# Optimization experiments

Measured on AMD Instinct MI355X. Metric: run time of the kernel, lower is better.

The kernel has to match this reference:

```python
import jax, jax.numpy as jnp
import numpy as np

# Pulse convention: bits[..., k] = bit k (LSB-first) of the IEEE-754 binary16 word.
# bits 0..9 = mantissa, bits 10..14 = exponent, bit 15 = sign.

def _encode_fp16(y16):
    """float16 array -> pulse bits [..., 16] in float32 {0,1}."""
    u = jax.lax.bitcast_convert_type(y16, jnp.uint16)
    k = jnp.arange(16, dtype=jnp.uint16)
    return ((u[..., None] >> k) & jnp.uint16(1)).astype(jnp.float32)

def _decode_fp16(bits):
    """Pulse bits [..., 16] -> exact fp16 value as float32 (arithmetic decode)."""
    pm = jnp.asarray([float(2 ** i) for i in range(10)], jnp.float32)
    pe = jnp.asarray([1.0, 2.0, 4.0, 8.0, 16.0], jnp.float32)
    m = bits[..., :10] @ pm          # mantissa integer [0, 1023]
    e = bits[..., 10:15] @ pe        # biased exponent [0, 31]
    s = 1.0 - 2.0 * bits[..., 15]    # sign
    frac = m * (1.0 / 1024.0)
    # normal: (-1)^s * 2^(e-15) * (1 + m/1024); subnormal (e==0): (-1)^s * 2^-14 * m/1024
    val = jnp.where(e > 0.0, jnp.exp2(e - 15.0) * (1.0 + frac), jnp.exp2(-14.0) * frac)
    return s * val

def setup_inputs() -> dict:
    key = jax.random.key(0)
    kx, kw = jax.random.split(key)
    B, T, IN, OUT = 4, 256, 512, 512
    x = jax.random.normal(kx, (B, T, IN), jnp.float32).astype(jnp.float16)
    w = (jax.random.normal(kw, (OUT, IN), jnp.float32) * (IN ** -0.5)).astype(jnp.float16)
    return {"x_pulse": _encode_fp16(x), "w_pulse": _encode_fp16(w)}

def reference(x_pulse, w_pulse):
    # x_pulse: [B, T, in, 16]; w_pulse: [out, in, 16]
    x_val = _decode_fp16(x_pulse)    # [B, T, in] exact fp16 values in fp32
    w_val = _decode_fp16(w_pulse)    # [out, in]
    # SpikeFP16MulToFP32: fp16*fp16 -> fp32 is exact (22-bit product fits fp32).
    # SequentialAccumulator: bit-exact deterministic O(n) fp32 add, i = 0..in-1.
    xs = (jnp.moveaxis(x_val, -1, 0), w_val.T)   # ([in, B, T], [in, out])
    acc0 = jnp.zeros(x_val.shape[:-1] + (w_val.shape[0],), jnp.float32)  # [B, T, out]
    def step(acc, xw):
        xi, wi = xw                   # [B, T], [out]
        return acc + xi[..., None] * wi, None
    acc, _ = jax.lax.scan(step, acc0, xs)
    # FP32ToFP16Converter (round-to-nearest-even) then re-encode to pulses.
    return _encode_fp16(acc.astype(jnp.float16))   # [B, T, out, 16]
```

## Files before the change

### kernel.cpp

```cpp
#include <hip/hip_runtime.h>
#include <hip/hip_fp16.h>

constexpr int K    = 512;
constexpr int ROWS = 1024;
constexpr int COLS = 512;
constexpr int NX   = ROWS * K;
constexpr int NW   = COLS * K;

__global__ __launch_bounds__(256) void decode_k(const float* __restrict__ xp,
                                                const float* __restrict__ wp,
                                                float* __restrict__ dec) {
    const int e = blockIdx.x * 256 + threadIdx.x;
    const float4* s4;
    if (e < NX) s4 = (const float4*)(xp + (size_t)e * 16);
    else        s4 = (const float4*)(wp + (size_t)(e - NX) * 16);
    const float4 v0 = s4[0];
    const float4 v1 = s4[1];
    const float4 v2 = s4[2];
    const float4 v3 = s4[3];
    unsigned u = 0;
    u |= (unsigned)(v0.x > 0.5f) << 0;
    u |= (unsigned)(v0.y > 0.5f) << 1;
    u |= (unsigned)(v0.z > 0.5f) << 2;
    u |= (unsigned)(v0.w > 0.5f) << 3;
    u |= (unsigned)(v1.x > 0.5f) << 4;
    u |= (unsigned)(v1.y > 0.5f) << 5;
    u |= (unsigned)(v1.z > 0.5f) << 6;
    u |= (unsigned)(v1.w > 0.5f) << 7;
    u |= (unsigned)(v2.x > 0.5f) << 8;
    u |= (unsigned)(v2.y > 0.5f) << 9;
    u |= (unsigned)(v2.z > 0.5f) << 10;
    u |= (unsigned)(v2.w > 0.5f) << 11;
    u |= (unsigned)(v3.x > 0.5f) << 12;
    u |= (unsigned)(v3.y > 0.5f) << 13;
    u |= (unsigned)(v3.z > 0.5f) << 14;
    u |= (unsigned)(v3.w > 0.5f) << 15;
    dec[e] = __half2float(__ushort_as_half((unsigned short)u));
}

__global__ __launch_bounds__(256) void gemm_k(const float* __restrict__ dec,
                                              float* __restrict__ out) {
    const float* __restrict__ xv = dec;
    const float* __restrict__ wv = dec + NX;

    __shared__ float Bs[64][68];

    const int tid  = threadIdx.x;
    const int lane = tid & 63;
    const int wid  = __builtin_amdgcn_readfirstlane(tid >> 6);
    const int col0 = blockIdx.x * 64;
    const int row0 = blockIdx.y * 32 + wid * 8;

    float acc[8] = {0.f, 0.f, 0.f, 0.f, 0.f, 0.f, 0.f, 0.f};

    const int scol = tid >> 2;
    const int skq  = (tid & 3) << 4;
    const float* wsrc = wv + (size_t)(col0 + scol) * K + skq;

    for (int k0 = 0; k0 < K; k0 += 64) {
        const float4 t0 = *(const float4*)(wsrc + k0 + 0);
        const float4 t1 = *(const float4*)(wsrc + k0 + 4);
        const float4 t2 = *(const float4*)(wsrc + k0 + 8);
        const float4 t3 = *(const float4*)(wsrc + k0 + 12);
        __syncthreads();
        *(float4*)&Bs[scol][skq + 0]  = t0;
        *(float4*)&Bs[scol][skq + 4]  = t1;
        *(float4*)&Bs[scol][skq + 8]  = t2;
        *(float4*)&Bs[scol][skq + 12] = t3;
        __syncthreads();

        const float* xbase = xv + k0;
        #pragma unroll
        for (int kc = 0; kc < 64; kc += 4) {
            const float4 b = *(const float4*)&Bs[lane][kc];
            #pragma unroll
            for (int r = 0; r < 8; ++r) {
                const float4 a = *(const float4*)(xbase + (size_t)(row0 + r) * K + kc);
                float s = acc[r];
                s = fmaf(a.x, b.x, s);
                s = fmaf(a.y, b.y, s);
                s = fmaf(a.z, b.z, s);
                s = fmaf(a.w, b.w, s);
                acc[r] = s;
            }
        }
    }

    #pragma unroll
    for (int r = 0; r < 8; ++r) {
        const unsigned short u = __half_as_ushort(__float2half_rn(acc[r]));
        float* o = out + ((size_t)(row0 + r) * COLS + (col0 + lane)) * 16;
        float4 q;
        q.x = (float)((u >> 0) & 1);
        q.y = (float)((u >> 1) & 1);
        q.z = (float)((u >> 2) & 1);
        q.w = (float)((u >> 3) & 1);
        *(float4*)(o + 0) = q;
        q.x = (float)((u >> 4) & 1);
        q.y = (float)((u >> 5) & 1);
        q.z = (float)((u >> 6) & 1);
        q.w = (float)((u >> 7) & 1);
        *(float4*)(o + 4) = q;
        q.x = (float)((u >> 8) & 1);
        q.y = (float)((u >> 9) & 1);
        q.z = (float)((u >> 10) & 1);
        q.w = (float)((u >> 11) & 1);
        *(float4*)(o + 8) = q;
        q.x = (float)((u >> 12) & 1);
        q.y = (float)((u >> 13) & 1);
        q.z = (float)((u >> 14) & 1);
        q.w = (float)((u >> 15) & 1);
        *(float4*)(o + 12) = q;
    }
}

extern "C" void kernel_launch(void* const* d_in, const int* in_sizes, int n_in,
                              void* d_out, int out_size, void* d_ws, size_t ws_size,
                              hipStream_t stream) {
    const float* xp = (const float*)d_in[0];
    const float* wp = (const float*)d_in[1];
    float* outp = (float*)d_out;
    float* dec  = (float*)d_ws;

    const int n_elem = NX + NW;
    decode_k<<<n_elem / 256, 256, 0, stream>>>(xp, wp, dec);

    dim3 grid(COLS / 64, ROWS / 32);
    gemm_k<<<grid, 256, 0, stream>>>(dec, outp);
}
```

Before: 149.0 us.

## Coalesce decode via LDS transpose and prefetch/register-block GEMM with smaller row tiles

The decode kernel now loads pulse data with coalesced float4 reads across the block, stages it in padded LDS, and extracts each bit from float exponent bit 23 instead of comparing. The GEMM halves rows per wave to 4, which doubles the grid for more parallelism. It also prefetches the next W tile into registers while the current tile is computed and preloads the B row and A chunks into register arrays. The per-row sequential accumulation order over k is kept. Larger register arrays (64 floats for b plus 64 for a) may raise VGPR pressure and lower occupancy.

```diff
diff --git a/kernel.cpp b/kernel.cpp
--- a/kernel.cpp
+++ b/kernel.cpp
@@ -10,32 +10,31 @@
 __global__ __launch_bounds__(256) void decode_k(const float* __restrict__ xp,
                                                 const float* __restrict__ wp,
                                                 float* __restrict__ dec) {
-    const int e = blockIdx.x * 256 + threadIdx.x;
-    const float4* s4;
-    if (e < NX) s4 = (const float4*)(xp + (size_t)e * 16);
-    else        s4 = (const float4*)(wp + (size_t)(e - NX) * 16);
-    const float4 v0 = s4[0];
-    const float4 v1 = s4[1];
-    const float4 v2 = s4[2];
-    const float4 v3 = s4[3];
+    __shared__ float lds[256 * 17];
+    const int t = threadIdx.x;
+    const int ebase = blockIdx.x << 8;
+    const float4* s4 = (ebase < NX)
+        ? (const float4*)(xp + (size_t)ebase * 16)
+        : (const float4*)(wp + (size_t)(ebase - NX) * 16);
+
+    #pragma unroll
+    for (int j = 0; j < 4; ++j) {
+        const int f = t + (j << 8);
+        const float4 v = s4[f];
+        const int e = f >> 2;
+        const int q = f & 3;
+        *(float4*)&lds[e * 17 + (q << 2)] = v;
+    }
+    __syncthreads();
+
+    const float* m = &lds[t * 17];
     unsigned u = 0;
-    u |= (unsigned)(v0.x > 0.5f) << 0;
-    u |= (unsigned)(v0.y > 0.5f) << 1;
-    u |= (unsigned)(v0.z > 0.5f) << 2;
-    u |= (unsigned)(v0.w > 0.5f) << 3;
-    u |= (unsigned)(v1.x > 0.5f) << 4;
-    u |= (unsigned)(v1.y > 0.5f) << 5;
-    u |= (unsigned)(v1.z > 0.5f) << 6;
-    u |= (unsigned)(v1.w > 0.5f) << 7;
-    u |= (unsigned)(v2.x > 0.5f) << 8;
-    u |= (unsigned)(v2.y > 0.5f) << 9;
-    u |= (unsigned)(v2.z > 0.5f) << 10;
-    u |= (unsigned)(v2.w > 0.5f) << 11;
-    u |= (unsigned)(v3.x > 0.5f) << 12;
-    u |= (unsigned)(v3.y > 0.5f) << 13;
-    u |= (unsigned)(v3.z > 0.5f) << 14;
-    u |= (unsigned)(v3.w > 0.5f) << 15;
-    dec[e] = __half2float(__ushort_as_half((unsigned short)u));
+    #pragma unroll
+    for (int k = 0; k < 16; ++k) {
+        const unsigned w = __float_as_uint(m[k]);
+        u |= ((w >> 23) & 1u) << k;
+    }
+    dec[ebase + t] = __half2float(__ushort_as_half((unsigned short)u));
 }
 
 __global__ __launch_bounds__(256) void gemm_k(const float* __restrict__ dec,
@@ -48,20 +47,23 @@
     const int tid  = threadIdx.x;
     const int lane = tid & 63;
     const int wid  = __builtin_amdgcn_readfirstlane(tid >> 6);
-    const int col0 = blockIdx.x * 64;
-    const int row0 = blockIdx.y * 32 + wid * 8;
+    const int col0 = blockIdx.x << 6;
+    const int row0 = (blockIdx.y << 4) + (wid << 2);
 
-    float acc[8] = {0.f, 0.f, 0.f, 0.f, 0.f, 0.f, 0.f, 0.f};
+    float acc[4] = {0.f, 0.f, 0.f, 0.f};
 
     const int scol = tid >> 2;
     const int skq  = (tid & 3) << 4;
     const float* wsrc = wv + (size_t)(col0 + scol) * K + skq;
 
+    float4 t0 = *(const float4*)(wsrc + 0);
+    float4 t1 = *(const float4*)(wsrc + 4);
+    float4 t2 = *(const float4*)(wsrc + 8);
+    float4 t3 = *(const float4*)(wsrc + 12);
+
+    const float* arow = xv + (size_t)row0 * K;
+
     for (int k0 = 0; k0 < K; k0 += 64) {
-        const float4 t0 = *(const float4*)(wsrc + k0 + 0);
-        const float4 t1 = *(const float4*)(wsrc + k0 + 4);
-        const float4 t2 = *(const float4*)(wsrc + k0 + 8);
-        const float4 t3 = *(const float4*)(wsrc + k0 + 12);
         __syncthreads();
         *(float4*)&Bs[scol][skq + 0]  = t0;
         *(float4*)&Bs[scol][skq + 4]  = t1;
@@ -69,25 +71,39 @@
         *(float4*)&Bs[scol][skq + 12] = t3;
         __syncthreads();
 
-        const float* xbase = xv + k0;
+        if (k0 + 64 < K) {
+            t0 = *(const float4*)(wsrc + k0 + 64 + 0);
+            t1 = *(const float4*)(wsrc + k0 + 64 + 4);
+            t2 = *(const float4*)(wsrc + k0 + 64 + 8);
+            t3 = *(const float4*)(wsrc + k0 + 64 + 12);
+        }
+
+        float b[64];
         #pragma unroll
-        for (int kc = 0; kc < 64; kc += 4) {
-            const float4 b = *(const float4*)&Bs[lane][kc];
+        for (int q = 0; q < 16; ++q)
+            *(float4*)&b[q * 4] = *(const float4*)&Bs[lane][q << 2];
+
+        #pragma unroll
+        for (int p = 0; p < 4; ++p) {
+            float a[4][16];
             #pragma unroll
-            for (int r = 0; r < 8; ++r) {
-                const float4 a = *(const float4*)(xbase + (size_t)(row0 + r) * K + kc);
-                float s = acc[r];
-                s = fmaf(a.x, b.x, s);
-                s = fmaf(a.y, b.y, s);
-                s = fmaf(a.z, b.z, s);
-                s = fmaf(a.w, b.w, s);
-                acc[r] = s;
+            for (int r = 0; r < 4; ++r) {
+                const float* ap = arow + (size_t)r * K + k0 + (p << 4);
+                #pragma unroll
+                for (int q = 0; q < 4; ++q)
+                    *(float4*)&a[r][q << 2] = *(const float4*)(ap + (q << 2));
+            }
+            #pragma unroll
+            for (int kk = 0; kk < 16; ++kk) {
+                #pragma unroll
+                for (int r = 0; r < 4; ++r)
+                    acc[r] = fmaf(a[r][kk], b[(p << 4) + kk], acc[r]);
             }
         }
     }
 
     #pragma unroll
-    for (int r = 0; r < 8; ++r) {
+    for (int r = 0; r < 4; ++r) {
         const unsigned short u = __half_as_ushort(__float2half_rn(acc[r]));
         float* o = out + ((size_t)(row0 + r) * COLS + (col0 + lane)) * 16;
         float4 q;
@@ -125,6 +141,6 @@
     const int n_elem = NX + NW;
     decode_k<<<n_elem / 256, 256, 0, stream>>>(xp, wp, dec);
 
-    dim3 grid(COLS / 64, ROWS / 32);
+    dim3 grid(COLS / 64, ROWS / 16);
     gemm_k<<<grid, 256, 0, stream>>>(dec, outp);
 }
```

Result: faster. 126.8 us (-14.9%).
